# Performance work log

Hardware: AMD Instinct MI355X
Metric: run time of the kernel (lower is better)

## Reference

```python
import jax, jax.numpy as jnp
import numpy as np

# dims: S=seq_len, E=nenv, H=max_human_num, D=human_embedding_size, A=attention_size, NH=heads
S, E, H, D, A, NH = 128, 256, 20, 64, 64, 8
NEG = -1e9


def setup_inputs() -> dict:
    key = jax.random.key(0)
    ks = jax.random.split(key, 9)
    sc = 1.0 / np.sqrt(D).astype(np.float32)
    return {
        "h_temporal": jax.random.normal(ks[0], (S, E, 1, D), jnp.float32),
        "h_spatials": jax.random.normal(ks[1], (S, E, H, D), jnp.float32),
        "each_seq_len": jax.random.randint(ks[2], (S * E,), 0, H, dtype=jnp.int32),
        # per-head Linear params, stored [in, out] (equivalent to torch y = x W^T + b)
        "Wt": jax.random.normal(ks[3], (NH, D, A), jnp.float32) * sc,
        "bt": jax.random.normal(ks[4], (NH, A), jnp.float32) * 0.01,
        "Ws": jax.random.normal(ks[5], (NH, D, A), jnp.float32) * sc,
        "bs": jax.random.normal(ks[6], (NH, A), jnp.float32) * 0.01,
        # final merge linear: concat over heads (NH*D) -> D
        "Wf": jax.random.normal(ks[7], (NH * D, D), jnp.float32) / np.sqrt(NH * D).astype(np.float32),
        "bf": jax.random.normal(ks[8], (D,), jnp.float32) * 0.01,
    }


def reference(h_temporal, h_spatials, each_seq_len, Wt, bt, Ws, bs, Wf, bf):
    s, e, h, d = h_spatials.shape
    a = Wt.shape[-1]
    nh = Wt.shape[0]

    # per-head embeddings (heads vectorized instead of python loop)
    # temporal: [s,e,1,d] -> [s,e,nh,a] (the size-1 edge dim is summed out == squeeze)
    te = jnp.einsum('seoh,nha->sena', h_temporal, Wt) + bt            # [s,e,nh,a]
    sp = jnp.einsum('semh,nha->senma', h_spatials, Ws) + bs[:, None]  # [s,e,nh,h,a]

    # elementwise-product scoring, summed over attention dim, scaled by num_edges/sqrt(A)
    temperature = h / np.sqrt(a).astype(np.float32)
    scores = jnp.einsum('sena,senma->senm', te, sp) * temperature     # [s,e,nh,h]

    # mask: True for neighbor index j < each_seq_len (cumsum-of-onehot trick, closed form)
    mask = (jnp.arange(h)[None, :] < each_seq_len[:, None]).reshape(s, e, h)
    scores = jnp.where(mask[:, :, None, :], scores, NEG)
    attn = jax.nn.softmax(scores, axis=-1)                            # [s,e,nh,h]

    # weighted sum of spatial hidden states (the tiny bmm), per head
    wv = jnp.einsum('senm,semh->senh', attn, h_spatials)              # [s,e,nh,d]

    # concat heads (head-major, matching torch.cat over last dim) + final merge linear
    out = wv.reshape(s, e, 1, nh * d) @ Wf + bf                       # [s,e,1,d]
    return out
```

## Files before the change

kernel.cpp:

```cpp
#include <hip/hip_runtime.h>
#include <hip/hip_bf16.h>

typedef __attribute__((ext_vector_type(8))) short short8;
typedef __attribute__((ext_vector_type(4))) float f32x4;

constexpr float TEMP = 2.5f;
constexpr float NEGV = -1e9f;

constexpr int K_OFF  = 0;
constexpr int P_OFF  = 512;
constexpr int Q_OFF  = 1024;
constexpr int PFRAG  = 1040;
constexpr int MFRAG  = 2064;
constexpr int WFRAG  = 34832;

constexpr int HS2_U   = 0;
constexpr int HS2_PL  = 11520;
constexpr int V2_U    = 23040;
constexpr int V2_PL   = 4672;
constexpr int HT2_U   = 32384;
constexpr int ATTP_F = 16832;
constexpr int C_F    = 17984;
constexpr int LEN_F  = 18048;
constexpr int LDS_FL = 18056;

#define MFMA_B16 __builtin_amdgcn_mfma_f32_16x16x32_bf16

__device__ inline ushort bf16_rne(float x) {
  uint u = __float_as_uint(x);
  u += 0x7FFF + ((u >> 16) & 1);
  return (ushort)(u >> 16);
}
__device__ inline float bf16_f(ushort h) { return __uint_as_float(((uint)h) << 16); }
__device__ inline void split2(float x, ushort& h0, ushort& h1) {
  h0 = bf16_rne(x);
  h1 = bf16_rne(x - bf16_f(h0));
}
__device__ inline ushort split_lvl2(float x, int s) {
  ushort h0 = bf16_rne(x);
  return s == 0 ? h0 : bf16_rne(x - bf16_f(h0));
}
__device__ inline uint pkbf16x2(float a, float b) {
  __hip_bfloat162 h = __float22bfloat162_rn(make_float2(a, b));
  uint u; __builtin_memcpy(&u, &h, 4);
  return u;
}
__device__ inline uint2 pkbf16x4(float4 v) {
  uint2 r; r.x = pkbf16x2(v.x, v.y); r.y = pkbf16x2(v.z, v.w);
  return r;
}
__device__ inline void pksplit4(float4 v, uint2& u0, uint2& u1) {
  u0 = pkbf16x4(v);
  float4 r;
  r.x = v.x - __uint_as_float(u0.x << 16);
  r.y = v.y - __uint_as_float(u0.x & 0xffff0000u);
  r.z = v.z - __uint_as_float(u0.y << 16);
  r.w = v.w - __uint_as_float(u0.y & 0xffff0000u);
  u1 = pkbf16x4(r);
}
__device__ inline short8 pack4(uint a, uint b, uint c, uint d) {
  union { uint u[4]; short8 s; } cv;
  cv.u[0] = a; cv.u[1] = b; cv.u[2] = c; cv.u[3] = d;
  return cv.s;
}

__global__ __launch_bounds__(256) void prep_kernel(
    const float* __restrict__ Wt, const float* __restrict__ bt,
    const float* __restrict__ Ws, const float* __restrict__ bs,
    const float* __restrict__ Wf, float* __restrict__ ws) {
  __shared__ float AL[64 * 65];
  __shared__ float BL[64 * 65];
  __shared__ float ML[64 * 65];
  const int t = threadIdx.x;
  uint* wsu = (uint*)ws;
  if (blockIdx.x < 8) {
    const int n = blockIdx.x;
#pragma unroll
    for (int i = 0; i < 16; ++i) {
      int idx = i * 256 + t;
      AL[(idx >> 6) * 65 + (idx & 63)] = Wt[n * 4096 + idx];
      BL[(idx >> 6) * 65 + (idx & 63)] = Ws[n * 4096 + idx];
    }
    __syncthreads();
#pragma unroll
    for (int i = 0; i < 16; ++i) {
      int idx = i * 256 + t;
      int dp = idx >> 6, d = idx & 63;
      float acc = 0.f;
#pragma unroll 8
      for (int a = 0; a < 64; ++a) acc += AL[dp * 65 + a] * BL[d * 65 + a];
      ML[dp * 65 + d] = acc * TEMP;
    }
    if (t < 64) {
      float acc = 0.f;
#pragma unroll 8
      for (int a = 0; a < 64; ++a) acc += BL[t * 65 + a] * bt[n * 64 + a];
      ws[K_OFF + n * 64 + t] = acc * TEMP;
    } else if (t < 128) {
      int r = t - 64;
      float acc = 0.f;
#pragma unroll 8
      for (int a = 0; a < 64; ++a) acc += AL[r * 65 + a] * bs[n * 64 + a];
      ws[P_OFF + n * 64 + r] = acc * TEMP;
    } else if (t == 128) {
      float acc = 0.f;
      for (int a = 0; a < 64; ++a) acc += bt[n * 64 + a] * bs[n * 64 + a];
      ws[Q_OFF + n] = acc * TEMP;
    }
    __syncthreads();
#pragma unroll
    for (int i = 0; i < 16; ++i) {
      int f = i * 256 + t;
      int r = f & 3, lane = (f >> 2) & 63, g = f >> 8;
      int s = g & 1, dt = (g >> 1) & 3, ks = g >> 3;
      int k = ks * 32 + ((lane >> 4) & 3) * 8 + r * 2;
      int d = dt * 16 + (lane & 15);
      uint lo = split_lvl2(ML[k * 65 + d], s);
      uint hi = split_lvl2(ML[(k + 1) * 65 + d], s);
      wsu[MFRAG + n * 4096 + (((ks * 4 + dt) * 2 + s) * 64 + lane) * 4 + r] =
          lo | (hi << 16);
    }
  } else if (blockIdx.x < 16) {
    const int n = blockIdx.x - 8;
#pragma unroll
    for (int i = 0; i < 16; ++i) {
      int idx = i * 256 + t;
      AL[(idx >> 6) * 65 + (idx & 63)] = Wf[(n * 64 + (idx >> 6)) * 64 + (idx & 63)];
    }
    __syncthreads();
#pragma unroll
    for (int i = 0; i < 8; ++i) {
      int f = i * 256 + t;
      int r = f & 3, lane = (f >> 2) & 63, g = f >> 8;
      int dt = g & 3, ks = g >> 2;
      int k = ks * 32 + ((lane >> 4) & 3) * 8 + r * 2;
      int d = dt * 16 + (lane & 15);
      uint lo = bf16_rne(AL[k * 65 + d]);
      uint hi = bf16_rne(AL[(k + 1) * 65 + d]);
      wsu[WFRAG + n * 2048 + ((ks * 4 + dt) * 64 + lane) * 4 + r] =
          lo | (hi << 16);
    }
  } else {
#pragma unroll
    for (int i = 0; i < 2; ++i) {
      int idx = i * 256 + t;
      int n = idx >> 6, dp = idx & 63;
      float acc = 0.f;
#pragma unroll 8
      for (int a = 0; a < 64; ++a)
        acc += Wt[n * 4096 + dp * 64 + a] * bs[n * 64 + a];
      AL[idx] = acc * TEMP;
    }
    __syncthreads();
#pragma unroll
    for (int i = 0; i < 4; ++i) {
      int f = i * 256 + t;
      int r = f & 3, lane = (f >> 2) & 63, g = f >> 8;
      int s = g & 1, ks = g >> 1;
      int k = ks * 32 + ((lane >> 4) & 3) * 8 + r * 2;
      int col = lane & 15;
      uint lo = (col < 8) ? (uint)split_lvl2(AL[col * 64 + k], s) : 0u;
      uint hi = (col < 8) ? (uint)split_lvl2(AL[col * 64 + k + 1], s) : 0u;
      wsu[PFRAG + ((ks * 2 + s) * 64 + lane) * 4 + r] = lo | (hi << 16);
    }
  }
}

#define SPLIT2_MFMA(FB, DT, CC)                                      \
  {                                                                  \
    short8 b00 = *(const short8*)&(FB)[((0 * 4 + (DT)) * 2 + 0) * 256]; \
    short8 b01 = *(const short8*)&(FB)[((0 * 4 + (DT)) * 2 + 1) * 256]; \
    short8 b10 = *(const short8*)&(FB)[((1 * 4 + (DT)) * 2 + 0) * 256]; \
    short8 b11 = *(const short8*)&(FB)[((1 * 4 + (DT)) * 2 + 1) * 256]; \
    CC = MFMA_B16(a00, b00, CC, 0, 0, 0);                            \
    CC = MFMA_B16(a10, b10, CC, 0, 0, 0);                            \
    CC = MFMA_B16(a00, b01, CC, 0, 0, 0);                            \
    CC = MFMA_B16(a01, b00, CC, 0, 0, 0);                            \
    CC = MFMA_B16(a10, b11, CC, 0, 0, 0);                            \
    CC = MFMA_B16(a11, b10, CC, 0, 0, 0);                            \
  }

#define LOAD_A(BASEU, ROWSTR, PLANESTR, ROW, KOFF)                   \
  short8 a00 = *(const short8*)&(BASEU)[(ROW) * (ROWSTR) + (KOFF)];               \
  short8 a01 = *(const short8*)&(BASEU)[(PLANESTR) + (ROW) * (ROWSTR) + (KOFF)];  \
  short8 a10 = *(const short8*)&(BASEU)[(ROW) * (ROWSTR) + 32 + (KOFF)];          \
  short8 a11 = *(const short8*)&(BASEU)[(PLANESTR) + (ROW) * (ROWSTR) + 32 + (KOFF)];

#define HV_LOAD(I, DST)                                                      \
  {                                                                          \
    const int f_ = (I) * 512 + t;                                            \
    const int p_ = f_ / 320;                                                 \
    const int s_ = f_ - p_ * 320;                                            \
    DST = *(const float4*)(hs_g + (size_t)(pair0 + p_) * 1280 +              \
                           (s_ >> 4) * 64 + (s_ & 15) * 4);                  \
  }
#define HV_STORE(I, SRC)                                                     \
  {                                                                          \
    const int f_ = (I) * 512 + t;                                            \
    const int p_ = f_ / 320;                                                 \
    const int s_ = f_ - p_ * 320;                                            \
    uint2 u0_, u1_; pksplit4(SRC, u0_, u1_);                                 \
    ushort* d_ = ldsu + HS2_U + p_ * 1440 + (s_ >> 4) * 72 + (s_ & 15) * 4;  \
    *(uint2*)d_ = u0_;                                                       \
    *(uint2*)(d_ + HS2_PL) = u1_;                                            \
  }

__global__ __launch_bounds__(512, 4) void attn_kernel(
    const float* __restrict__ ht_g, const float* __restrict__ hs_g,
    const int* __restrict__ len_g, const float* __restrict__ bf,
    const float* __restrict__ wsp, float* __restrict__ out) {
  __shared__ __align__(16) float lds[LDS_FL];
  ushort* ldsu = (ushort*)lds;
  const int t    = threadIdx.x;
  const int lane = t & 63;
  const int w    = t >> 6;
  const int pair0 = blockIdx.x * 8;
  const uint* wsu = (const uint*)wsp;
  const int lo4 = lane & 15, kg = lane >> 4;
  const int rp8 = lo4 & 7;
  const int dtw = w & 3, ngw = w >> 2;

  short8 wfB0[4], wfB1[4];
#pragma unroll
  for (int nn = 0; nn < 4; ++nn) {
    const uint* fb = wsu + WFRAG + (ngw * 4 + nn) * 2048 + lane * 4;
    wfB0[nn] = *(const short8*)&fb[(0 * 4 + dtw) * 256];
    wfB1[nn] = *(const short8*)&fb[(1 * 4 + dtw) * 256];
  }

  {
    float x = ht_g[(size_t)pair0 * 64 + t];
    ushort h0, h1; split2(x, h0, h1);
    const int p = t >> 6, dp = t & 63;
    ldsu[HT2_U + 0 * 640 + p * 80 + dp] = h0;
    ldsu[HT2_U + 1 * 640 + p * 80 + dp] = h1;
  }
  if (t < 8) lds[LEN_F + t] = (float)len_g[pair0 + t];
  __syncthreads();

  float4 hv0, hv1, hv2, hv3, hv4;

  {
    const int n = w;
    LOAD_A(ldsu + HT2_U, 80, 640, rp8, kg * 8)
    const uint* fb = wsu + MFRAG + n * 4096 + lane * 4;
    const float* kb = &wsp[K_OFF + n * 64 + lo4];
    float kv0 = kb[0], kv1 = kb[16], kv2 = kb[32], kv3 = kb[48];
    f32x4 c0 = {kv0, kv0, kv0, kv0};
    f32x4 c1 = {kv1, kv1, kv1, kv1};
    f32x4 c2 = {kv2, kv2, kv2, kv2};
    f32x4 c3 = {kv3, kv3, kv3, kv3};
    __builtin_amdgcn_s_setprio(1);
    SPLIT2_MFMA(fb, 0, c0)
    SPLIT2_MFMA(fb, 1, c1)
    SPLIT2_MFMA(fb, 2, c2)
    SPLIT2_MFMA(fb, 3, c3)
    __builtin_amdgcn_s_setprio(0);

    HV_LOAD(0, hv0) HV_LOAD(1, hv1) HV_LOAD(2, hv2) HV_LOAD(3, hv3) HV_LOAD(4, hv4)

    if (kg < 2) {
#pragma unroll
      for (int reg = 0; reg < 4; ++reg) {
        const int p = kg * 4 + reg;
        ushort* vp = ldsu + V2_U + p * 584 + n * 72 + lo4;
        ushort h0, h1;
        split2(c0[reg], h0, h1); vp[0]  = h0; vp[V2_PL]      = h1;
        split2(c1[reg], h0, h1); vp[16] = h0; vp[V2_PL + 16] = h1;
        split2(c2[reg], h0, h1); vp[32] = h0; vp[V2_PL + 32] = h1;
        split2(c3[reg], h0, h1); vp[48] = h0; vp[V2_PL + 48] = h1;
      }
    }
  }

  if (w == 0) {
    LOAD_A(ldsu + HT2_U, 80, 640, rp8, kg * 8)
    const uint* fbp = wsu + PFRAG + lane * 4;
    short8 b00 = *(const short8*)&fbp[0 * 256];
    short8 b01 = *(const short8*)&fbp[1 * 256];
    short8 b10 = *(const short8*)&fbp[2 * 256];
    short8 b11 = *(const short8*)&fbp[3 * 256];
    float qv = (lo4 < 8) ? wsp[Q_OFF + lo4] : 0.f;
    f32x4 cc = {qv, qv, qv, qv};
    cc = MFMA_B16(a00, b00, cc, 0, 0, 0);
    cc = MFMA_B16(a10, b10, cc, 0, 0, 0);
    cc = MFMA_B16(a00, b01, cc, 0, 0, 0);
    cc = MFMA_B16(a01, b00, cc, 0, 0, 0);
    cc = MFMA_B16(a10, b11, cc, 0, 0, 0);
    cc = MFMA_B16(a11, b10, cc, 0, 0, 0);
    if (kg < 2 && lo4 < 8) {
#pragma unroll
      for (int reg = 0; reg < 4; ++reg)
        lds[C_F + (kg * 4 + reg) * 8 + lo4] = cc[reg];
    }
  }

  HV_STORE(0, hv0) HV_STORE(1, hv1) HV_STORE(2, hv2) HV_STORE(3, hv3) HV_STORE(4, hv4)
  __syncthreads();

  {
    const int p = w;
    const int n8 = rp8;
    const int lenp = (int)lds[LEN_F + p];
    const ushort* vb = ldsu + V2_U + p * 584 + n8 * 72;
    const short8 B00 = *(const short8*)&vb[kg * 8];
    const short8 B01 = *(const short8*)&vb[V2_PL + kg * 8];
    const short8 B10 = *(const short8*)&vb[32 + kg * 8];
    const short8 B11 = *(const short8*)&vb[V2_PL + 32 + kg * 8];
    const float cv = lds[C_F + p * 8 + n8];
    f32x4 acc0 = {cv, cv, cv, cv};
    f32x4 acc1 = {cv, cv, cv, cv};
    __builtin_amdgcn_s_setprio(1);
    {
      const ushort* ab = ldsu + HS2_U + p * 1440;
      LOAD_A(ab, 72, HS2_PL, lo4, kg * 8)
      acc0 = MFMA_B16(a00, B00, acc0, 0, 0, 0);
      acc0 = MFMA_B16(a10, B10, acc0, 0, 0, 0);
      acc0 = MFMA_B16(a00, B01, acc0, 0, 0, 0);
      acc0 = MFMA_B16(a01, B00, acc0, 0, 0, 0);
      acc0 = MFMA_B16(a10, B11, acc0, 0, 0, 0);
      acc0 = MFMA_B16(a11, B10, acc0, 0, 0, 0);
    }
    {
      const int row = (16 + lo4 < 20) ? (16 + lo4) : 19;
      const ushort* ab = ldsu + HS2_U + p * 1440;
      LOAD_A(ab, 72, HS2_PL, row, kg * 8)
      acc1 = MFMA_B16(a00, B00, acc1, 0, 0, 0);
      acc1 = MFMA_B16(a10, B10, acc1, 0, 0, 0);
      acc1 = MFMA_B16(a00, B01, acc1, 0, 0, 0);
      acc1 = MFMA_B16(a01, B00, acc1, 0, 0, 0);
      acc1 = MFMA_B16(a10, B11, acc1, 0, 0, 0);
      acc1 = MFMA_B16(a11, B10, acc1, 0, 0, 0);
    }
    __builtin_amdgcn_s_setprio(0);
    float e0[4], e1[4];
    float mx = NEGV;
#pragma unroll
    for (int r = 0; r < 4; ++r) {
      const int m0 = kg * 4 + r;
      const int m1 = 16 + kg * 4 + r;
      e0[r] = (m0 < lenp) ? acc0[r] : NEGV;
      e1[r] = (m1 < lenp) ? acc1[r] : NEGV;
      mx = fmaxf(mx, fmaxf(e0[r], e1[r]));
    }
    mx = fmaxf(mx, __shfl_xor(mx, 16));
    mx = fmaxf(mx, __shfl_xor(mx, 32));
    float sm = 0.f;
#pragma unroll
    for (int r = 0; r < 4; ++r) {
      e0[r] = __expf(e0[r] - mx);
      e1[r] = (kg == 0) ? __expf(e1[r] - mx) : 0.f;
      sm += e0[r] + e1[r];
    }
    sm += __shfl_xor(sm, 16);
    sm += __shfl_xor(sm, 32);
    const float inv = 1.0f / sm;
    uint* attp = (uint*)&lds[ATTP_F] + p * 144;
    if (lo4 < 8) {
      attp[(kg * 2 + 0) * 9 + lo4] = pkbf16x2(e0[0] * inv, e0[1] * inv);
      attp[(kg * 2 + 1) * 9 + lo4] = pkbf16x2(e0[2] * inv, e0[3] * inv);
      if (kg == 0) {
        attp[8 * 9 + lo4] = pkbf16x2(e1[0] * inv, e1[1] * inv);
        attp[9 * 9 + lo4] = pkbf16x2(e1[2] * inv, e1[3] * inv);
      } else if (kg == 1) {
        attp[14 * 9 + lo4] = 0u; attp[15 * 9 + lo4] = 0u;
      } else if (kg == 2) {
        attp[10 * 9 + lo4] = 0u; attp[11 * 9 + lo4] = 0u;
      } else {
        attp[12 * 9 + lo4] = 0u; attp[13 * 9 + lo4] = 0u;
      }
    }
  }

  {
    const int p = w;
    const uint* attp = (const uint*)&lds[ATTP_F] + p * 144;
    const ushort* hsb = ldsu + HS2_U + p * 1440;
    uint a_[4];
#pragma unroll
    for (int r = 0; r < 4; ++r)
      a_[r] = attp[(kg * 4 + r) * 9 + rp8];
    const short8 A = pack4(a_[0], a_[1], a_[2], a_[3]);
    ushort* wp = ldsu + V2_U + p * 584;
#pragma unroll
    for (int dt = 0; dt < 4; ++dt) {
      uint b_[4];
#pragma unroll
      for (int r = 0; r < 4; ++r) {
        const int m0 = kg * 8 + 2 * r;
        const int d = dt * 16 + lo4;
        uint blo = (m0 < 20) ? (uint)hsb[m0 * 72 + d] : 0u;
        uint bhi = (m0 + 1 < 20) ? (uint)hsb[(m0 + 1) * 72 + d] : 0u;
        b_[r] = blo | (bhi << 16);
      }
      const short8 B = pack4(b_[0], b_[1], b_[2], b_[3]);
      f32x4 cc = {0.f, 0.f, 0.f, 0.f};
      cc = MFMA_B16(A, B, cc, 0, 0, 0);
      if (kg < 2) {
#pragma unroll
        for (int reg = 0; reg < 4; ++reg) {
          const int n = kg * 4 + reg;
          wp[n * 72 + dt * 16 + lo4] = bf16_rne(cc[reg]);
        }
      }
    }
  }
  __syncthreads();

  {
    f32x4 cc = {0.f, 0.f, 0.f, 0.f};
#pragma unroll
    for (int nn = 0; nn < 4; ++nn) {
      const int n = ngw * 4 + nn;
      const ushort* ab = ldsu + V2_U + rp8 * 584 + n * 72;
      const short8 a0 = *(const short8*)&ab[kg * 8];
      const short8 a1 = *(const short8*)&ab[32 + kg * 8];
      cc = MFMA_B16(a0, wfB0[nn], cc, 0, 0, 0);
      cc = MFMA_B16(a1, wfB1[nn], cc, 0, 0, 0);
    }
    if (kg < 2) {
#pragma unroll
      for (int reg = 0; reg < 4; ++reg)
        lds[0 + ngw * 512 + (kg * 4 + reg) * 64 + dtw * 16 + lo4] = cc[reg];
    }
  }
  __syncthreads();

  {
    const int d = t & 63;
    out[(size_t)pair0 * 64 + t] = bf[d] + lds[t] + lds[512 + t];
  }
}

extern "C" void kernel_launch(void* const* d_in, const int* in_sizes, int n_in,
                              void* d_out, int out_size, void* d_ws, size_t ws_size,
                              hipStream_t stream) {
  const float* ht  = (const float*)d_in[0];
  const float* hs  = (const float*)d_in[1];
  const int*   len = (const int*)d_in[2];
  const float* Wt  = (const float*)d_in[3];
  const float* bt  = (const float*)d_in[4];
  const float* Ws  = (const float*)d_in[5];
  const float* bs  = (const float*)d_in[6];
  const float* Wf  = (const float*)d_in[7];
  const float* bf  = (const float*)d_in[8];
  float* outp = (float*)d_out;
  float* ws   = (float*)d_ws;

  hipLaunchKernelGGL(prep_kernel, dim3(17), dim3(256), 0, stream,
                     Wt, bt, Ws, bs, Wf, ws);
  hipLaunchKernelGGL(attn_kernel, dim3(4096), dim3(512), 0, stream,
                     ht, hs, len, bf, ws, outp);
}
```

Before: 85.32 us.

## Halve block size to four pairs per 256-thread block

Each block now handles 4 (seq,env) pairs with 4 waves instead of 8 pairs with 8 waves, and the grid is doubled. Each wave computes two heads in the embedding step and both head-groups in the final merge. The Wf fragments are now loaded inside the merge loop instead of being preloaded into registers. The LDS footprint per block halves, which should allow more resident blocks and finer scheduling. The cost is that the MFMA M-dimension is only partly used (4 of 16 rows valid), so a larger share of MFMA work is wasted.

```diff
diff --git a/kernel.cpp b/kernel.cpp
--- a/kernel.cpp
+++ b/kernel.cpp
@@ -15,14 +15,14 @@
 constexpr int WFRAG  = 34832;
 
 constexpr int HS2_U   = 0;
-constexpr int HS2_PL  = 11520;
-constexpr int V2_U    = 23040;
-constexpr int V2_PL   = 4672;
-constexpr int HT2_U   = 32384;
-constexpr int ATTP_F = 16832;
-constexpr int C_F    = 17984;
-constexpr int LEN_F  = 18048;
-constexpr int LDS_FL = 18056;
+constexpr int HS2_PL  = 5760;
+constexpr int V2_U    = 11520;
+constexpr int V2_PL   = 2336;
+constexpr int HT2_U   = 16192;
+constexpr int ATTP_F = 8416;
+constexpr int C_F    = 8992;
+constexpr int LEN_F  = 9024;
+constexpr int LDS_FL = 9028;
 
 #define MFMA_B16 __builtin_amdgcn_mfma_f32_16x16x32_bf16
 
@@ -188,7 +188,7 @@
 
 #define HV_LOAD(I, DST)                                                      \
   {                                                                          \
-    const int f_ = (I) * 512 + t;                                            \
+    const int f_ = (I) * 256 + t;                                            \
     const int p_ = f_ / 320;                                                 \
     const int s_ = f_ - p_ * 320;                                            \
     DST = *(const float4*)(hs_g + (size_t)(pair0 + p_) * 1280 +              \
@@ -196,7 +196,7 @@
   }
 #define HV_STORE(I, SRC)                                                     \
   {                                                                          \
-    const int f_ = (I) * 512 + t;                                            \
+    const int f_ = (I) * 256 + t;                                            \
     const int p_ = f_ / 320;                                                 \
     const int s_ = f_ - p_ * 320;                                            \
     uint2 u0_, u1_; pksplit4(SRC, u0_, u1_);                                 \
@@ -205,7 +205,7 @@
     *(uint2*)(d_ + HS2_PL) = u1_;                                            \
   }
 
-__global__ __launch_bounds__(512, 4) void attn_kernel(
+__global__ __launch_bounds__(256, 4) void attn_kernel(
     const float* __restrict__ ht_g, const float* __restrict__ hs_g,
     const int* __restrict__ len_g, const float* __restrict__ bf,
     const float* __restrict__ wsp, float* __restrict__ out) {
@@ -214,67 +214,64 @@
   const int t    = threadIdx.x;
   const int lane = t & 63;
   const int w    = t >> 6;
-  const int pair0 = blockIdx.x * 8;
+  const int pair0 = blockIdx.x * 4;
   const uint* wsu = (const uint*)wsp;
   const int lo4 = lane & 15, kg = lane >> 4;
   const int rp8 = lo4 & 7;
-  const int dtw = w & 3, ngw = w >> 2;
-
-  short8 wfB0[4], wfB1[4];
-#pragma unroll
-  for (int nn = 0; nn < 4; ++nn) {
-    const uint* fb = wsu + WFRAG + (ngw * 4 + nn) * 2048 + lane * 4;
-    wfB0[nn] = *(const short8*)&fb[(0 * 4 + dtw) * 256];
-    wfB1[nn] = *(const short8*)&fb[(1 * 4 + dtw) * 256];
-  }
+  const int rp4 = lo4 & 3;
+  const int dtw = w;
 
   {
     float x = ht_g[(size_t)pair0 * 64 + t];
     ushort h0, h1; split2(x, h0, h1);
     const int p = t >> 6, dp = t & 63;
-    ldsu[HT2_U + 0 * 640 + p * 80 + dp] = h0;
-    ldsu[HT2_U + 1 * 640 + p * 80 + dp] = h1;
-  }
-  if (t < 8) lds[LEN_F + t] = (float)len_g[pair0 + t];
+    ldsu[HT2_U + 0 * 320 + p * 80 + dp] = h0;
+    ldsu[HT2_U + 1 * 320 + p * 80 + dp] = h1;
+  }
+  if (t < 4) lds[LEN_F + t] = (float)len_g[pair0 + t];
   __syncthreads();
 
   float4 hv0, hv1, hv2, hv3, hv4;
 
   {
-    const int n = w;
-    LOAD_A(ldsu + HT2_U, 80, 640, rp8, kg * 8)
-    const uint* fb = wsu + MFRAG + n * 4096 + lane * 4;
-    const float* kb = &wsp[K_OFF + n * 64 + lo4];
-    float kv0 = kb[0], kv1 = kb[16], kv2 = kb[32], kv3 = kb[48];
-    f32x4 c0 = {kv0, kv0, kv0, kv0};
-    f32x4 c1 = {kv1, kv1, kv1, kv1};
-    f32x4 c2 = {kv2, kv2, kv2, kv2};
-    f32x4 c3 = {kv3, kv3, kv3, kv3};
-    __builtin_amdgcn_s_setprio(1);
-    SPLIT2_MFMA(fb, 0, c0)
-    SPLIT2_MFMA(fb, 1, c1)
-    SPLIT2_MFMA(fb, 2, c2)
-    SPLIT2_MFMA(fb, 3, c3)
-    __builtin_amdgcn_s_setprio(0);
-
-    HV_LOAD(0, hv0) HV_LOAD(1, hv1) HV_LOAD(2, hv2) HV_LOAD(3, hv3) HV_LOAD(4, hv4)
-
-    if (kg < 2) {
-#pragma unroll
-      for (int reg = 0; reg < 4; ++reg) {
-        const int p = kg * 4 + reg;
-        ushort* vp = ldsu + V2_U + p * 584 + n * 72 + lo4;
-        ushort h0, h1;
-        split2(c0[reg], h0, h1); vp[0]  = h0; vp[V2_PL]      = h1;
-        split2(c1[reg], h0, h1); vp[16] = h0; vp[V2_PL + 16] = h1;
-        split2(c2[reg], h0, h1); vp[32] = h0; vp[V2_PL + 32] = h1;
-        split2(c3[reg], h0, h1); vp[48] = h0; vp[V2_PL + 48] = h1;
+    LOAD_A(ldsu + HT2_U, 80, 320, rp4, kg * 8)
+#pragma unroll
+    for (int h = 0; h < 2; ++h) {
+      const int n = 2 * w + h;
+      const uint* fb = wsu + MFRAG + n * 4096 + lane * 4;
+      const float* kb = &wsp[K_OFF + n * 64 + lo4];
+      float kv0 = kb[0], kv1 = kb[16], kv2 = kb[32], kv3 = kb[48];
+      f32x4 c0 = {kv0, kv0, kv0, kv0};
+      f32x4 c1 = {kv1, kv1, kv1, kv1};
+      f32x4 c2 = {kv2, kv2, kv2, kv2};
+      f32x4 c3 = {kv3, kv3, kv3, kv3};
+      __builtin_amdgcn_s_setprio(1);
+      SPLIT2_MFMA(fb, 0, c0)
+      SPLIT2_MFMA(fb, 1, c1)
+      SPLIT2_MFMA(fb, 2, c2)
+      SPLIT2_MFMA(fb, 3, c3)
+      __builtin_amdgcn_s_setprio(0);
+
+      if (h == 1) {
+        HV_LOAD(0, hv0) HV_LOAD(1, hv1) HV_LOAD(2, hv2)
+        HV_LOAD(3, hv3) HV_LOAD(4, hv4)
+      }
+      if (kg == 0) {
+#pragma unroll
+        for (int reg = 0; reg < 4; ++reg) {
+          ushort* vp = ldsu + V2_U + reg * 584 + n * 72 + lo4;
+          ushort h0_, h1_;
+          split2(c0[reg], h0_, h1_); vp[0]  = h0_; vp[V2_PL]      = h1_;
+          split2(c1[reg], h0_, h1_); vp[16] = h0_; vp[V2_PL + 16] = h1_;
+          split2(c2[reg], h0_, h1_); vp[32] = h0_; vp[V2_PL + 32] = h1_;
+          split2(c3[reg], h0_, h1_); vp[48] = h0_; vp[V2_PL + 48] = h1_;
+        }
       }
     }
   }
 
   if (w == 0) {
-    LOAD_A(ldsu + HT2_U, 80, 640, rp8, kg * 8)
+    LOAD_A(ldsu + HT2_U, 80, 320, rp4, kg * 8)
     const uint* fbp = wsu + PFRAG + lane * 4;
     short8 b00 = *(const short8*)&fbp[0 * 256];
     short8 b01 = *(const short8*)&fbp[1 * 256];
@@ -288,10 +285,10 @@
     cc = MFMA_B16(a01, b00, cc, 0, 0, 0);
     cc = MFMA_B16(a10, b11, cc, 0, 0, 0);
     cc = MFMA_B16(a11, b10, cc, 0, 0, 0);
-    if (kg < 2 && lo4 < 8) {
+    if (kg == 0 && lo4 < 8) {
 #pragma unroll
       for (int reg = 0; reg < 4; ++reg)
-        lds[C_F + (kg * 4 + reg) * 8 + lo4] = cc[reg];
+        lds[C_F + reg * 8 + lo4] = cc[reg];
     }
   }
 
@@ -408,27 +405,33 @@
   __syncthreads();
 
   {
-    f32x4 cc = {0.f, 0.f, 0.f, 0.f};
-#pragma unroll
-    for (int nn = 0; nn < 4; ++nn) {
-      const int n = ngw * 4 + nn;
-      const ushort* ab = ldsu + V2_U + rp8 * 584 + n * 72;
-      const short8 a0 = *(const short8*)&ab[kg * 8];
-      const short8 a1 = *(const short8*)&ab[32 + kg * 8];
-      cc = MFMA_B16(a0, wfB0[nn], cc, 0, 0, 0);
-      cc = MFMA_B16(a1, wfB1[nn], cc, 0, 0, 0);
-    }
-    if (kg < 2) {
-#pragma unroll
-      for (int reg = 0; reg < 4; ++reg)
-        lds[0 + ngw * 512 + (kg * 4 + reg) * 64 + dtw * 16 + lo4] = cc[reg];
+#pragma unroll
+    for (int ng = 0; ng < 2; ++ng) {
+      f32x4 cc = {0.f, 0.f, 0.f, 0.f};
+#pragma unroll
+      for (int nn = 0; nn < 4; ++nn) {
+        const int n = ng * 4 + nn;
+        const ushort* ab = ldsu + V2_U + rp4 * 584 + n * 72;
+        const short8 a0 = *(const short8*)&ab[kg * 8];
+        const short8 a1 = *(const short8*)&ab[32 + kg * 8];
+        const uint* fb = wsu + WFRAG + n * 2048 + lane * 4;
+        const short8 b0 = *(const short8*)&fb[(0 * 4 + dtw) * 256];
+        const short8 b1 = *(const short8*)&fb[(1 * 4 + dtw) * 256];
+        cc = MFMA_B16(a0, b0, cc, 0, 0, 0);
+        cc = MFMA_B16(a1, b1, cc, 0, 0, 0);
+      }
+      if (kg == 0) {
+#pragma unroll
+        for (int reg = 0; reg < 4; ++reg)
+          lds[0 + ng * 256 + reg * 64 + dtw * 16 + lo4] = cc[reg];
+      }
     }
   }
   __syncthreads();
 
   {
     const int d = t & 63;
-    out[(size_t)pair0 * 64 + t] = bf[d] + lds[t] + lds[512 + t];
+    out[(size_t)pair0 * 64 + t] = bf[d] + lds[t] + lds[256 + t];
   }
 }
 
@@ -449,6 +452,6 @@
 
   hipLaunchKernelGGL(prep_kernel, dim3(17), dim3(256), 0, stream,
                      Wt, bt, Ws, bs, Wf, ws);
-  hipLaunchKernelGGL(attn_kernel, dim3(4096), dim3(512), 0, stream,
+  hipLaunchKernelGGL(attn_kernel, dim3(8192), dim3(256), 0, stream,
                      ht, hs, len, bf, ws, outp);
 }
```

After: 107.1 us. 25.5% more time.
